# Performance work log

Measured on AMD Instinct MI355X. Metric: run time of the kernel, lower is better.

## Reference

```python
import jax, jax.numpy as jnp
import numpy as np

N_NODES = 50000
N_EDGES = 800000
D_IN = 64
D_OUT = 64


def setup_inputs() -> dict:
    key = jax.random.key(0)
    k1, k2, k3, k4, k5, k6 = jax.random.split(key, 6)
    stdv = 1.0 / np.sqrt(D_OUT)
    return {
        "X": jax.random.normal(k1, (N_NODES, D_IN), dtype=jnp.float32),
        "edge_src": jax.random.randint(k2, (N_EDGES,), 0, N_NODES, dtype=jnp.int32),
        "edge_dst": jax.random.randint(k3, (N_EDGES,), 0, N_NODES, dtype=jnp.int32),
        "edge_weight": jax.random.uniform(k4, (N_EDGES,), dtype=jnp.float32),
        "weight": jax.random.uniform(k5, (D_IN, D_OUT), jnp.float32, -stdv, stdv),
        "b": jax.random.uniform(k6, (D_OUT,), jnp.float32, -stdv, stdv),
    }


def reference(X, edge_src, edge_dst, edge_weight, weight, b):
    # support = X @ W                        [N, D_OUT]
    support = jnp.dot(X, weight)
    # spmm: out[d] = sum_{e: dst(e)=d} w_e * support[src(e)]
    messages = edge_weight[:, None] * support[edge_src]  # [E, D_OUT]
    output = jax.ops.segment_sum(messages, edge_dst, num_segments=N_NODES)
    return output + b
```

## Files before the change

### kernel.cpp

```cpp
#include <hip/hip_runtime.h>
#include <hip/hip_bf16.h>

#define N_NODES 50000
#define N_EDGES 800000
#define DIM     64
#define CAP     64

#define GEMM_BLOCKS ((N_NODES + 63) / 64)
#define FILL_BLOCKS ((N_EDGES / 4 + 255) / 256)

#define WS_SUPPORT  0
#define WS_CURSOR   6400000
#define WS_BUCKET   9600000

__device__ inline unsigned bf16_hi(float f) {
    const unsigned u = __float_as_uint(f);
    return (u + 0x7fffu + ((u >> 16) & 1u)) & 0xffff0000u;
}

__global__ __launch_bounds__(256) void fused_gemm_fill_kernel(
        const float* __restrict__ X,
        const float* __restrict__ W,
        ushort* __restrict__ support,
        const int*   __restrict__ edge_src,
        const int*   __restrict__ edge_dst,
        const float* __restrict__ edge_weight,
        int*      __restrict__ cursor,
        unsigned* __restrict__ bucket) {
    const int bid = blockIdx.x >> 1;
    const int tid = threadIdx.x;

    if (blockIdx.x & 1) {
        const int base = (bid * 256 + tid) * 4;
        if (base < N_EDGES) {
            const int4   d = *(const int4*)  &edge_dst[base];
            const int4   s = *(const int4*)  &edge_src[base];
            const float4 w = *(const float4*)&edge_weight[base];
            const unsigned e0 = bf16_hi(w.x) | (unsigned)s.x;
            const unsigned e1 = bf16_hi(w.y) | (unsigned)s.y;
            const unsigned e2 = bf16_hi(w.z) | (unsigned)s.z;
            const unsigned e3 = bf16_hi(w.w) | (unsigned)s.w;
            const int p0 = atomicAdd(&cursor[d.x << 4], 1);
            const int p1 = atomicAdd(&cursor[d.y << 4], 1);
            const int p2 = atomicAdd(&cursor[d.z << 4], 1);
            const int p3 = atomicAdd(&cursor[d.w << 4], 1);
            if (p0 < CAP) bucket[d.x * CAP + p0] = e0;
            if (p1 < CAP) bucket[d.y * CAP + p1] = e1;
            if (p2 < CAP) bucket[d.z * CAP + p2] = e2;
            if (p3 < CAP) bucket[d.w * CAP + p3] = e3;
        }
        return;
    }

    __shared__ float sX[64 * 68];
    __shared__ float sW[64 * 64];
    const int rowBase = bid * 64;

    #pragma unroll
    for (int i = 0; i < 4; ++i) {
        const int q   = tid + 256 * i;
        const int row = q >> 4;
        const int c4  = q & 15;
        float4 v = make_float4(0.f, 0.f, 0.f, 0.f);
        if (rowBase + row < N_NODES)
            v = *(const float4*)&X[(rowBase + row) * DIM + c4 * 4];
        *(float4*)&sX[row * 68 + c4 * 4] = v;
    }
    #pragma unroll
    for (int i = 0; i < 4; ++i) {
        const int q   = tid + 256 * i;
        const int row = q >> 4;
        const int c4  = q & 15;
        *(float4*)&sW[row * 64 + c4 * 4] = *(const float4*)&W[row * DIM + c4 * 4];
    }
    __syncthreads();

    const int tx = tid & 15;
    const int ty = tid >> 4;
    float acc[4][4];
    #pragma unroll
    for (int i = 0; i < 4; ++i)
        #pragma unroll
        for (int j = 0; j < 4; ++j) acc[i][j] = 0.f;

    #pragma unroll
    for (int k4 = 0; k4 < 16; ++k4) {
        float4 xv[4], wv[4];
        #pragma unroll
        for (int i = 0; i < 4; ++i)
            xv[i] = *(const float4*)&sX[(ty * 4 + i) * 68 + k4 * 4];
        #pragma unroll
        for (int kk = 0; kk < 4; ++kk)
            wv[kk] = *(const float4*)&sW[(k4 * 4 + kk) * 64 + tx * 4];
        #pragma unroll
        for (int i = 0; i < 4; ++i) {
            #pragma unroll
            for (int kk = 0; kk < 4; ++kk) {
                const float f = ((const float*)&xv[i])[kk];
                acc[i][0] += f * wv[kk].x;
                acc[i][1] += f * wv[kk].y;
                acc[i][2] += f * wv[kk].z;
                acc[i][3] += f * wv[kk].w;
            }
        }
    }

    #pragma unroll
    for (int i = 0; i < 4; ++i) {
        const int r = rowBase + ty * 4 + i;
        if (r < N_NODES) {
            ushort4 v;
            v.x = __hip_bfloat16_raw(__float2bfloat16(acc[i][0])).x;
            v.y = __hip_bfloat16_raw(__float2bfloat16(acc[i][1])).x;
            v.z = __hip_bfloat16_raw(__float2bfloat16(acc[i][2])).x;
            v.w = __hip_bfloat16_raw(__float2bfloat16(acc[i][3])).x;
            *(ushort4*)&support[r * DIM + tx * 4] = v;
        }
    }
}

__global__ __launch_bounds__(256) void gather_kernel(const int*      __restrict__ cursor,
                                                     const unsigned* __restrict__ bucket,
                                                     const ushort*   __restrict__ support,
                                                     const float*    __restrict__ b,
                                                     float* __restrict__ out) {
    const int node = blockIdx.x * 4 + (threadIdx.x >> 6);
    const int lane = threadIdx.x & 63;
    if (node >= N_NODES) return;

    int cnt = cursor[node << 4];
    if (cnt > CAP) cnt = CAP;
    const unsigned* bk = &bucket[node * CAP];

    float acc = 0.f;
    int j = 0;
    for (; j + 4 <= cnt; j += 4) {
        const uint4 e = *(const uint4*)&bk[j];
        const int   s0 = (int)(e.x & 0xffffu);
        const int   s1 = (int)(e.y & 0xffffu);
        const int   s2 = (int)(e.z & 0xffffu);
        const int   s3 = (int)(e.w & 0xffffu);
        const float w0 = __uint_as_float(e.x & 0xffff0000u);
        const float w1 = __uint_as_float(e.y & 0xffff0000u);
        const float w2 = __uint_as_float(e.z & 0xffff0000u);
        const float w3 = __uint_as_float(e.w & 0xffff0000u);
        const float v0 = __uint_as_float((unsigned)support[s0 * DIM + lane] << 16);
        const float v1 = __uint_as_float((unsigned)support[s1 * DIM + lane] << 16);
        const float v2 = __uint_as_float((unsigned)support[s2 * DIM + lane] << 16);
        const float v3 = __uint_as_float((unsigned)support[s3 * DIM + lane] << 16);
        acc += w0 * v0;
        acc += w1 * v1;
        acc += w2 * v2;
        acc += w3 * v3;
    }
    for (; j < cnt; ++j) {
        const unsigned e = bk[j];
        const int   s = (int)(e & 0xffffu);
        const float w = __uint_as_float(e & 0xffff0000u);
        acc += w * __uint_as_float((unsigned)support[s * DIM + lane] << 16);
    }
    out[node * DIM + lane] = acc + b[lane];
}

extern "C" void kernel_launch(void* const* d_in, const int* in_sizes, int n_in,
                              void* d_out, int out_size, void* d_ws, size_t ws_size,
                              hipStream_t stream) {
    const float* X           = (const float*)d_in[0];
    const int*   edge_src    = (const int*)  d_in[1];
    const int*   edge_dst    = (const int*)  d_in[2];
    const float* edge_weight = (const float*)d_in[3];
    const float* W           = (const float*)d_in[4];
    const float* b           = (const float*)d_in[5];
    float*       out         = (float*)d_out;

    char* ws = (char*)d_ws;
    ushort*   support = (ushort*)  (ws + WS_SUPPORT);
    int*      cursor  = (int*)     (ws + WS_CURSOR);
    unsigned* bucket  = (unsigned*)(ws + WS_BUCKET);

    hipMemsetAsync(cursor, 0, N_NODES * 16 * sizeof(int), stream);

    hipLaunchKernelGGL(fused_gemm_fill_kernel, dim3(GEMM_BLOCKS + FILL_BLOCKS),
                       dim3(256), 0, stream,
                       X, W, support, edge_src, edge_dst, edge_weight,
                       cursor, bucket);

    hipLaunchKernelGGL(gather_kernel, dim3(N_NODES / 4), dim3(256), 0, stream,
                       cursor, bucket, support, b, out);
}
```

Baseline: 148.7 us.

## Partition edge fill by XCD destination range and broadcast bucket entries via shuffles

The edge-fill phase now launches 8 blocks per 2048-edge chunk, one per XCD (taken as blockIdx & 7). Each block filters edges to its own destination-node range, so the cursor atomics and bucket writes for a node stay within one XCD's L2. The cost is that edge_dst is read eight times and the src/weight reads become scalar. The GEMM tile shrinks to 32 rows with a launch-bounds occupancy hint. In the gather, each lane loads one bucket entry and the entries are broadcast with __shfl instead of every lane reloading uint4s.

```diff
diff --git a/kernel.cpp b/kernel.cpp
--- a/kernel.cpp
+++ b/kernel.cpp
@@ -6,8 +6,11 @@
 #define DIM     64
 #define CAP     64
 
-#define GEMM_BLOCKS ((N_NODES + 63) / 64)
-#define FILL_BLOCKS ((N_EDGES / 4 + 255) / 256)
+#define NODES_PER_XCD (N_NODES / 8)
+#define CHUNK_E       2048
+#define FILL_CHUNKS   ((N_EDGES + CHUNK_E - 1) / CHUNK_E)
+#define FILL_TOTAL    (FILL_CHUNKS * 8)
+#define GEMM_BLOCKS   ((N_NODES + 31) / 32)
 
 #define WS_SUPPORT  0
 #define WS_CURSOR   6400000
@@ -18,7 +21,7 @@
     return (u + 0x7fffu + ((u >> 16) & 1u)) & 0xffff0000u;
 }
 
-__global__ __launch_bounds__(256) void fused_gemm_fill_kernel(
+__global__ __launch_bounds__(256, 4) void fused_gemm_fill_kernel(
         const float* __restrict__ X,
         const float* __restrict__ W,
         ushort* __restrict__ support,
@@ -27,37 +30,38 @@
         const float* __restrict__ edge_weight,
         int*      __restrict__ cursor,
         unsigned* __restrict__ bucket) {
-    const int bid = blockIdx.x >> 1;
     const int tid = threadIdx.x;
 
-    if (blockIdx.x & 1) {
-        const int base = (bid * 256 + tid) * 4;
-        if (base < N_EDGES) {
-            const int4   d = *(const int4*)  &edge_dst[base];
-            const int4   s = *(const int4*)  &edge_src[base];
-            const float4 w = *(const float4*)&edge_weight[base];
-            const unsigned e0 = bf16_hi(w.x) | (unsigned)s.x;
-            const unsigned e1 = bf16_hi(w.y) | (unsigned)s.y;
-            const unsigned e2 = bf16_hi(w.z) | (unsigned)s.z;
-            const unsigned e3 = bf16_hi(w.w) | (unsigned)s.w;
-            const int p0 = atomicAdd(&cursor[d.x << 4], 1);
-            const int p1 = atomicAdd(&cursor[d.y << 4], 1);
-            const int p2 = atomicAdd(&cursor[d.z << 4], 1);
-            const int p3 = atomicAdd(&cursor[d.w << 4], 1);
-            if (p0 < CAP) bucket[d.x * CAP + p0] = e0;
-            if (p1 < CAP) bucket[d.y * CAP + p1] = e1;
-            if (p2 < CAP) bucket[d.z * CAP + p2] = e2;
-            if (p3 < CAP) bucket[d.w * CAP + p3] = e3;
+    if (blockIdx.x < FILL_TOTAL) {
+        const int xcd   = blockIdx.x & 7;
+        const int chunk = blockIdx.x >> 3;
+        const int lo    = xcd * NODES_PER_XCD;
+        const int hi    = lo + NODES_PER_XCD;
+        const int base  = chunk * CHUNK_E + tid * 8;
+        if (base + 8 <= N_EDGES) {
+            int d[8];
+            *(int4*)&d[0] = *(const int4*)&edge_dst[base];
+            *(int4*)&d[4] = *(const int4*)&edge_dst[base + 4];
+            #pragma unroll
+            for (int i = 0; i < 8; ++i) {
+                if (d[i] >= lo && d[i] < hi) {
+                    const int      e   = base + i;
+                    const unsigned ent = bf16_hi(edge_weight[e]) | (unsigned)edge_src[e];
+                    const int      p   = atomicAdd(&cursor[d[i] << 4], 1);
+                    if (p < CAP) bucket[d[i] * CAP + p] = ent;
+                }
+            }
         }
         return;
     }
 
-    __shared__ float sX[64 * 68];
+    __shared__ float sX[32 * 68];
     __shared__ float sW[64 * 64];
-    const int rowBase = bid * 64;
+    const int bid = blockIdx.x - FILL_TOTAL;
+    const int rowBase = bid * 32;
 
     #pragma unroll
-    for (int i = 0; i < 4; ++i) {
+    for (int i = 0; i < 2; ++i) {
         const int q   = tid + 256 * i;
         const int row = q >> 4;
         const int c4  = q & 15;
@@ -77,23 +81,23 @@
 
     const int tx = tid & 15;
     const int ty = tid >> 4;
-    float acc[4][4];
+    float acc[2][4];
     #pragma unroll
-    for (int i = 0; i < 4; ++i)
+    for (int i = 0; i < 2; ++i)
         #pragma unroll
         for (int j = 0; j < 4; ++j) acc[i][j] = 0.f;
 
     #pragma unroll
     for (int k4 = 0; k4 < 16; ++k4) {
-        float4 xv[4], wv[4];
+        float4 xv[2], wv[4];
         #pragma unroll
-        for (int i = 0; i < 4; ++i)
-            xv[i] = *(const float4*)&sX[(ty * 4 + i) * 68 + k4 * 4];
+        for (int i = 0; i < 2; ++i)
+            xv[i] = *(const float4*)&sX[(ty * 2 + i) * 68 + k4 * 4];
         #pragma unroll
         for (int kk = 0; kk < 4; ++kk)
             wv[kk] = *(const float4*)&sW[(k4 * 4 + kk) * 64 + tx * 4];
         #pragma unroll
-        for (int i = 0; i < 4; ++i) {
+        for (int i = 0; i < 2; ++i) {
             #pragma unroll
             for (int kk = 0; kk < 4; ++kk) {
                 const float f = ((const float*)&xv[i])[kk];
@@ -106,8 +110,8 @@
     }
 
     #pragma unroll
-    for (int i = 0; i < 4; ++i) {
-        const int r = rowBase + ty * 4 + i;
+    for (int i = 0; i < 2; ++i) {
+        const int r = rowBase + ty * 2 + i;
         if (r < N_NODES) {
             ushort4 v;
             v.x = __hip_bfloat16_raw(__float2bfloat16(acc[i][0])).x;
@@ -130,34 +134,28 @@
 
     int cnt = cursor[node << 4];
     if (cnt > CAP) cnt = CAP;
-    const unsigned* bk = &bucket[node * CAP];
+    const unsigned ent = bucket[node * CAP + lane];
 
     float acc = 0.f;
     int j = 0;
     for (; j + 4 <= cnt; j += 4) {
-        const uint4 e = *(const uint4*)&bk[j];
-        const int   s0 = (int)(e.x & 0xffffu);
-        const int   s1 = (int)(e.y & 0xffffu);
-        const int   s2 = (int)(e.z & 0xffffu);
-        const int   s3 = (int)(e.w & 0xffffu);
-        const float w0 = __uint_as_float(e.x & 0xffff0000u);
-        const float w1 = __uint_as_float(e.y & 0xffff0000u);
-        const float w2 = __uint_as_float(e.z & 0xffff0000u);
-        const float w3 = __uint_as_float(e.w & 0xffff0000u);
-        const float v0 = __uint_as_float((unsigned)support[s0 * DIM + lane] << 16);
-        const float v1 = __uint_as_float((unsigned)support[s1 * DIM + lane] << 16);
-        const float v2 = __uint_as_float((unsigned)support[s2 * DIM + lane] << 16);
-        const float v3 = __uint_as_float((unsigned)support[s3 * DIM + lane] << 16);
-        acc += w0 * v0;
-        acc += w1 * v1;
-        acc += w2 * v2;
-        acc += w3 * v3;
+        const unsigned e0 = __shfl(ent, j);
+        const unsigned e1 = __shfl(ent, j + 1);
+        const unsigned e2 = __shfl(ent, j + 2);
+        const unsigned e3 = __shfl(ent, j + 3);
+        const float v0 = __uint_as_float((unsigned)support[(e0 & 0xffffu) * DIM + lane] << 16);
+        const float v1 = __uint_as_float((unsigned)support[(e1 & 0xffffu) * DIM + lane] << 16);
+        const float v2 = __uint_as_float((unsigned)support[(e2 & 0xffffu) * DIM + lane] << 16);
+        const float v3 = __uint_as_float((unsigned)support[(e3 & 0xffffu) * DIM + lane] << 16);
+        acc += __uint_as_float(e0 & 0xffff0000u) * v0;
+        acc += __uint_as_float(e1 & 0xffff0000u) * v1;
+        acc += __uint_as_float(e2 & 0xffff0000u) * v2;
+        acc += __uint_as_float(e3 & 0xffff0000u) * v3;
     }
     for (; j < cnt; ++j) {
-        const unsigned e = bk[j];
-        const int   s = (int)(e & 0xffffu);
-        const float w = __uint_as_float(e & 0xffff0000u);
-        acc += w * __uint_as_float((unsigned)support[s * DIM + lane] << 16);
+        const unsigned e = __shfl(ent, j);
+        const float    v = __uint_as_float((unsigned)support[(e & 0xffffu) * DIM + lane] << 16);
+        acc += __uint_as_float(e & 0xffff0000u) * v;
     }
     out[node * DIM + lane] = acc + b[lane];
 }
@@ -180,7 +178,7 @@
 
     hipMemsetAsync(cursor, 0, N_NODES * 16 * sizeof(int), stream);
 
-    hipLaunchKernelGGL(fused_gemm_fill_kernel, dim3(GEMM_BLOCKS + FILL_BLOCKS),
+    hipLaunchKernelGGL(fused_gemm_fill_kernel, dim3(FILL_TOTAL + GEMM_BLOCKS),
                        dim3(256), 0, stream,
                        X, W, support, edge_src, edge_dst, edge_weight,
                        cursor, bucket);
```

Result: slower. 348.6 us (+134.4%).
